# Kernel tuning notes

Measured on AMD Instinct MI355X. Metric: run time of the kernel, lower is better.

Reference implementation:

```python
import jax, jax.numpy as jnp
import numpy as np

B, N, D = 8, 2048, 16   # batch, n_points, n_dim (num_df == D)
K, DM = 32, 256         # k neighbors, d_model


def setup_inputs() -> dict:
    key = jax.random.key(0)
    k0, k1, k2, k3, k4, k5 = jax.random.split(key, 6)
    x = jax.random.normal(k0, (B, N, D), jnp.float32)
    features = jax.random.uniform(k1, (B, D), jnp.float32)
    # nn.Linear(k, d_model, bias=False) weights: [out, in] = [DM, K]
    lim = 1.0 / np.sqrt(K)
    W_crd = jax.random.uniform(k2, (DM, K), jnp.float32, -lim, lim)
    W_ftr = jax.random.uniform(k3, (DM, K), jnp.float32, -lim, lim)
    pe_crd = 0.01 * jax.random.normal(k4, (1, 1, D, DM), jnp.float32)
    pe_ftr = 0.01 * jax.random.normal(k5, (1, 1, D, DM), jnp.float32)
    return {"x": x, "features": features, "W_crd": W_crd, "W_ftr": W_ftr,
            "pe_crd": pe_crd, "pe_ftr": pe_ftr, "k": K}


def _forward(x, features, W_crd, W_ftr, pe_crd, pe_ftr, k):
    b, n, d = x.shape
    # split coordinates vs features per-dimension
    fmask = features[:, None, :] > 0.1                 # [B,1,D]
    x_crd = jnp.where(fmask, 0.0, x)                   # masked_fill(features_, 0)
    x_ftr = jnp.where(fmask, x, 0.0)                   # masked_fill(~features_, 0)
    xc = jnp.concatenate([x_crd, x_ftr], axis=-1)      # [B,N,2D]
    # masked stats with attn_mask=None -> plain mean / unbiased std over points
    mean = jnp.mean(xc, axis=1, keepdims=True)
    std = jnp.std(xc, axis=1, keepdims=True, ddof=1)
    xc = jnp.clip((xc - mean) / (std + 1e-5), -10.0, 10.0)
    # pairwise L2 distances on coordinate part (torch.cdist, p=2)
    sq = jnp.sum(x_crd * x_crd, axis=-1)               # [B,N]
    d2 = sq[:, :, None] + sq[:, None, :] - 2.0 * jnp.einsum('bnd,bmd->bnm', x_crd, x_crd)
    dist = jnp.sqrt(jnp.maximum(d2, 0.0))              # [B,N,N]
    # k nearest neighbors (smallest distance, self included)
    _, idx = jax.lax.top_k(-dist, k)                   # [B,N,k]
    nb = xc[jnp.arange(b)[:, None, None], idx]         # gather neighbors [B,N,k,2D]
    local = nb - xc[:, :, None, :]                     # project_local: center frame
    xk = jnp.transpose(local, (0, 1, 3, 2))            # flatten=False -> [B,N,2D,k]
    crd, ftr = xk[:, :, :d, :], xk[:, :, d:, :]
    o_crd = (jnp.einsum('bnpk,dk->bnpd', crd, W_crd) + pe_crd).sum(axis=2)
    o_ftr = (jnp.einsum('bnpk,dk->bnpd', ftr, W_ftr) + pe_ftr).sum(axis=2)
    pe_loss = jnp.abs(pe_crd).sum() + jnp.abs(pe_ftr).sum()
    # dropout is identity in eval mode
    return o_crd + o_ftr, pe_loss


def reference(x, features, W_crd, W_ftr, pe_crd, pe_ftr, k):
    return _forward(x, features, W_crd, W_ftr, pe_crd, pe_ftr, k)
```

## Files before the change

### kernel.cpp

```cpp
#include <hip/hip_runtime.h>
#include <stdint.h>

#define B 8
#define N 2048
#define D 16
#define KNN 32
#define DM 256
#define CAP 128

__global__ __launch_bounds__(256) void knn_prep(
    const float* __restrict__ x, const float* __restrict__ features,
    const float* __restrict__ Wc, const float* __restrict__ Wf,
    const float* __restrict__ pec, const float* __restrict__ pef,
    float* __restrict__ xcrdT, float* __restrict__ sq,
    float* __restrict__ Tc, float* __restrict__ Tf,
    float* __restrict__ WcT, float* __restrict__ WfT,
    float* __restrict__ cbias, float* __restrict__ pe_loss_out)
{
    if (blockIdx.x == 64) {
        int dm = threadIdx.x;
        float cb = 0.f, al = 0.f;
#pragma unroll
        for (int p = 0; p < D; ++p)
            cb += pec[p * DM + dm] + pef[p * DM + dm];
#pragma unroll
        for (int p = 0; p < D; ++p)
            al += fabsf(pec[p * DM + dm]) + fabsf(pef[p * DM + dm]);
        cbias[dm] = cb;
#pragma unroll
        for (int k = 0; k < KNN; ++k) {
            WcT[k * DM + dm] = Wc[dm * KNN + k];
            WfT[k * DM + dm] = Wf[dm * KNN + k];
        }
        __shared__ float redf[256];
        redf[dm] = al; __syncthreads();
        for (int st = 128; st > 0; st >>= 1) {
            if (dm < st) redf[dm] += redf[dm + st];
            __syncthreads();
        }
        if (dm == 0) pe_loss_out[0] = redf[0];
        return;
    }

    int tid = threadIdx.x;
    int b = blockIdx.x >> 3;

    double ls[D], lq[D];
#pragma unroll
    for (int d = 0; d < D; ++d) { ls[d] = 0.0; lq[d] = 0.0; }
    for (int r = 0; r < 8; ++r) {
        const float* row = x + ((size_t)b * N + r * 256 + tid) * D;
#pragma unroll
        for (int d = 0; d < D; d += 4) {
            float4 v = *(const float4*)(row + d);
            double x0 = v.x, x1 = v.y, x2 = v.z, x3 = v.w;
            ls[d]   += x0; lq[d]   += x0 * x0;
            ls[d+1] += x1; lq[d+1] += x1 * x1;
            ls[d+2] += x2; lq[d+2] += x2 * x2;
            ls[d+3] += x3; lq[d+3] += x3 * x3;
        }
    }
#pragma unroll
    for (int d = 0; d < D; ++d) {
        double s = ls[d], q = lq[d];
#pragma unroll
        for (int st = 32; st >= 1; st >>= 1) {
            s += __shfl_xor(s, st, 64);
            q += __shfl_xor(q, st, 64);
        }
        ls[d] = s; lq[d] = q;
    }
    __shared__ double sred[4][2 * D];
    __shared__ float smean[32], sscale[32];
    int wave = tid >> 6, lane = tid & 63;
    if (lane == 0) {
#pragma unroll
        for (int d = 0; d < D; ++d) {
            sred[wave][d]     = ls[d];
            sred[wave][D + d] = lq[d];
        }
    }
    __syncthreads();
    if (tid < D) {
        int d = tid;
        double S = sred[0][d] + sred[1][d] + sred[2][d] + sred[3][d];
        double Q = sred[0][D+d] + sred[1][D+d] + sred[2][D+d] + sred[3][D+d];
        double mean = S / (double)N;
        double var  = (Q - S * S / (double)N) / (double)(N - 1);
        if (var < 0.0) var = 0.0;
        float stdv = (float)sqrt(var);
        float scl  = 1.0f / (stdv + 1e-5f);
        float scl0 = 1.0f / (0.0f + 1e-5f);
        bool mask = features[b * D + d] > 0.1f;
        smean [d]      = mask ? 0.0f : (float)mean;
        sscale[d]      = mask ? scl0 : scl;
        smean [16 + d] = mask ? (float)mean : 0.0f;
        sscale[16 + d] = mask ? scl : scl0;
    }
    __syncthreads();

    int t = blockIdx.x * 256 + tid;
    int nn = t & (N - 1);
    float tc = 0.f, tf = 0.f, s = 0.f;
    float row[D];
#pragma unroll
    for (int d = 0; d < D; ++d) {
        float xv = x[(size_t)t * D + d];
        bool mask = features[b * D + d] > 0.1f;
        float xc = mask ? 0.f : xv;
        float xf = mask ? xv : 0.f;
        row[d] = xc;
        s += xc * xc;
        float vc = (xc - smean[d])      * sscale[d];
        vc = fminf(10.f, fmaxf(-10.f, vc));
        float vf = (xf - smean[16 + d]) * sscale[16 + d];
        vf = fminf(10.f, fmaxf(-10.f, vf));
        tc += vc; tf += vf;
    }
#pragma unroll
    for (int d = 0; d < D; ++d)
        xcrdT[((size_t)b * D + d) * N + nn] = row[d];
    sq[t] = s; Tc[t] = tc; Tf[t] = tf;
}

#define WAVE_LDS_FENCE() do {                                   \
    asm volatile("s_waitcnt lgkmcnt(0)" ::: "memory");          \
    __builtin_amdgcn_sched_barrier(0);                          \
} while (0)

__global__ __launch_bounds__(256) void knn_main(
    const float* __restrict__ xcrdT, const float* __restrict__ sq,
    const float* __restrict__ Tc, const float* __restrict__ Tf,
    const float* __restrict__ WcT, const float* __restrict__ WfT,
    const float* __restrict__ cbias, float* __restrict__ out)
{
    __shared__ float tile[D][256];
    __shared__ unsigned long long collect[8][CAP];
    __shared__ int sortedm[8][KNN];
    __shared__ float akbk[8][KNN][2];

    const int tid  = threadIdx.x;
    const int lane = tid & 63;
    const int wid  = tid >> 6;
    const int qid0 = blockIdx.x * 8 + wid * 2;
    const int b  = qid0 >> 11;
    const int n0 = qid0 & (N - 1);
    const int n1 = n0 + 1;
    const int c0 = wid * 2, c1 = c0 + 1;

    const float* xbT = xcrdT + (size_t)b * D * N;
    const float* sqb = sq + b * N;

    float qx0[D], qx1[D];
#pragma unroll
    for (int d = 0; d < D; ++d) {
        float2 v = *(const float2*)(xbT + (size_t)d * N + n0);
        qx0[d] = v.x; qx1[d] = v.y;
    }
    const float sqn0 = sqb[n0], sqn1 = sqb[n1];

    float orig0[KNN], orig1[KNN];
    float vm0 = 1e30f, vm1 = 1e30f;
#pragma unroll
    for (int t = 0; t < 8; ++t) {
        __syncthreads();
        {
            const float* src = xbT + (size_t)(wid * 4) * N + t * 256 + lane * 4;
#pragma unroll
            for (int dd = 0; dd < 4; ++dd) {
                float4 v = *(const float4*)(src + (size_t)dd * N);
                *(float4*)&tile[wid * 4 + dd][lane * 4] = v;
            }
        }
        __syncthreads();
#pragma unroll
        for (int jt = 0; jt < 4; ++jt) {
            const int j  = t * 4 + jt;
            const int ml = jt * 64 + lane;
            float dot0 = 0.f, dot1 = 0.f;
#pragma unroll
            for (int d = 0; d < D; ++d) {
                float v = tile[d][ml];
                dot0 += qx0[d] * v;
                dot1 += qx1[d] * v;
            }
            float sm = sqb[t * 256 + ml];
            float o0 = fabsf(sqrtf(fmaxf(sqn0 + sm - 2.0f * dot0, 0.f)));
            float o1 = fabsf(sqrtf(fmaxf(sqn1 + sm - 2.0f * dot1, 0.f)));
            orig0[j] = o0; orig1[j] = o1;
            vm0 = fminf(vm0, o0); vm1 = fminf(vm1, o1);
        }
    }

#pragma unroll
    for (int k = 2; k <= 64; k <<= 1) {
#pragma unroll
        for (int j = k >> 1; j >= 1; j >>= 1) {
            float o0 = __shfl_xor(vm0, j, 64);
            float o1 = __shfl_xor(vm1, j, 64);
            bool lower = (lane & j) == 0;
            bool up    = (lane & k) == 0;
            vm0 = (lower == up) ? fminf(vm0, o0) : fmaxf(vm0, o0);
            vm1 = (lower == up) ? fminf(vm1, o1) : fmaxf(vm1, o1);
        }
    }
    const float tau0 = __shfl(vm0, 31, 64);
    const float tau1 = __shfl(vm1, 31, 64);

    const unsigned long long lmask = (1ULL << lane) - 1ULL;
    int T0, T1;
    {
        int base = 0;
#pragma unroll
        for (int j = 0; j < KNN; ++j) {
            bool f = (orig0[j] <= tau0);
            unsigned long long mk = __ballot(f);
            if (f) {
                int pos = base + (int)__popcll(mk & lmask);
                if (pos < CAP)
                    collect[c0][pos] =
                        (((unsigned long long)__float_as_uint(orig0[j])) << 11)
                        | (unsigned)(j * 64 + lane);
            }
            base += (int)__popcll(mk);
        }
        T0 = base < CAP ? base : CAP;
    }
    {
        int base = 0;
#pragma unroll
        for (int j = 0; j < KNN; ++j) {
            bool f = (orig1[j] <= tau1);
            unsigned long long mk = __ballot(f);
            if (f) {
                int pos = base + (int)__popcll(mk & lmask);
                if (pos < CAP)
                    collect[c1][pos] =
                        (((unsigned long long)__float_as_uint(orig1[j])) << 11)
                        | (unsigned)(j * 64 + lane);
            }
            base += (int)__popcll(mk);
        }
        T1 = base < CAP ? base : CAP;
    }
    WAVE_LDS_FENCE();

    if (T0 <= 64 && T1 <= 64) {
        unsigned long long key0 = (lane < T0) ? collect[c0][lane] : ~0ULL;
        unsigned long long key1 = (lane < T1) ? collect[c1][lane] : ~0ULL;
#pragma unroll
        for (int k = 2; k <= 64; k <<= 1) {
#pragma unroll
            for (int j = k >> 1; j >= 1; j >>= 1) {
                unsigned long long o0 = __shfl_xor(key0, j, 64);
                unsigned long long o1 = __shfl_xor(key1, j, 64);
                bool lower = (lane & j) == 0;
                bool up    = (lane & k) == 0;
                unsigned long long mn0 = (o0 < key0) ? o0 : key0;
                unsigned long long mx0 = (o0 < key0) ? key0 : o0;
                unsigned long long mn1 = (o1 < key1) ? o1 : key1;
                unsigned long long mx1 = (o1 < key1) ? key1 : o1;
                key0 = (lower == up) ? mn0 : mx0;
                key1 = (lower == up) ? mn1 : mx1;
            }
        }
        if (lane < KNN) {
            sortedm[c0][lane] = (int)(key0 & 2047u);
            sortedm[c1][lane] = (int)(key1 & 2047u);
        }
    } else {
#pragma unroll 1
        for (int q = 0; q < 2; ++q) {
            int T = q ? T1 : T0;
            unsigned long long* co = collect[q ? c1 : c0];
            int* so = sortedm[q ? c1 : c0];
            if (T <= 64) {
                unsigned long long key = (lane < T) ? co[lane] : ~0ULL;
#pragma unroll
                for (int k = 2; k <= 64; k <<= 1) {
#pragma unroll
                    for (int j = k >> 1; j >= 1; j >>= 1) {
                        unsigned long long o = __shfl_xor(key, j, 64);
                        bool lower = (lane & j) == 0;
                        bool up    = (lane & k) == 0;
                        unsigned long long mn = (o < key) ? o : key;
                        unsigned long long mx = (o < key) ? key : o;
                        key = (lower == up) ? mn : mx;
                    }
                }
                if (lane < KNN) so[lane] = (int)(key & 2047u);
            } else {
#pragma unroll 1
                for (int slot = 0; slot < CAP / 64; ++slot) {
                    int i = lane + slot * 64;
                    if (i < T) {
                        unsigned long long mk = co[i];
                        int rank = 0;
#pragma unroll 4
                        for (int t2 = 0; t2 < T; ++t2)
                            rank += (co[t2] < mk) ? 1 : 0;
                        if (rank < KNN) so[rank] = (int)(mk & 2047u);
                    }
                }
            }
        }
    }
    WAVE_LDS_FENCE();

    const float* Tcb = Tc + b * N;
    const float* Tfb = Tf + b * N;
    {
        const float Tcn0 = Tcb[n0], Tfn0 = Tfb[n0];
        const float Tcn1 = Tcb[n1], Tfn1 = Tfb[n1];
        int q = lane >> 5;
        int k = lane & 31;
        int wm = sortedm[c0 + q][k];
        float av = Tcb[wm] - (q ? Tcn1 : Tcn0);
        float bv = Tfb[wm] - (q ? Tfn1 : Tfn0);
        akbk[c0 + q][k][0] = av;
        akbk[c0 + q][k][1] = bv;
    }
    WAVE_LDS_FENCE();

    float acc0[4] = {0.f, 0.f, 0.f, 0.f};
    float acc1[4] = {0.f, 0.f, 0.f, 0.f};

#pragma unroll
    for (int k = 0; k < KNN; ++k) {
        float ak0 = akbk[c0][k][0], bk0 = akbk[c0][k][1];
        float ak1 = akbk[c1][k][0], bk1 = akbk[c1][k][1];
        const float* wc = WcT + k * DM + lane;
        const float* wf = WfT + k * DM + lane;
#pragma unroll
        for (int q = 0; q < 4; ++q) {
            float wcv = wc[q * 64];
            float wfv = wf[q * 64];
            acc0[q] += wcv * ak0 + wfv * bk0;
            acc1[q] += wcv * ak1 + wfv * bk1;
        }
    }

    size_t ob0 = (size_t)qid0 * DM + lane;
#pragma unroll
    for (int q = 0; q < 4; ++q) {
        float cb = cbias[lane + q * 64];
        out[ob0 + q * 64]      = acc0[q] + cb;
        out[ob0 + DM + q * 64] = acc1[q] + cb;
    }
}

extern "C" void kernel_launch(void* const* d_in, const int* in_sizes, int n_in,
                              void* d_out, int out_size, void* d_ws, size_t ws_size,
                              hipStream_t stream)
{
    const float* x        = (const float*)d_in[0];
    const float* features = (const float*)d_in[1];
    const float* W_crd    = (const float*)d_in[2];
    const float* W_ftr    = (const float*)d_in[3];
    const float* pe_crd   = (const float*)d_in[4];
    const float* pe_ftr   = (const float*)d_in[5];

    float* out = (float*)d_out;

    float* xcrdT = (float*)d_ws;
    float* sqv   = xcrdT + (size_t)B * N * D;
    float* Tc    = sqv  + B * N;
    float* Tf    = Tc   + B * N;
    float* cbias = Tf   + B * N;
    float* WcT   = cbias + DM;
    float* WfT   = WcT + KNN * DM;

    knn_prep<<<65, 256, 0, stream>>>(x, features, W_crd, W_ftr, pe_crd, pe_ftr,
                                     xcrdT, sqv, Tc, Tf, WcT, WfT, cbias,
                                     out + (size_t)out_size - 1);
    knn_main<<<(B * N) / 8, 256, 0, stream>>>(xcrdT, sqv, Tc, Tf,
                                              WcT, WfT, cbias, out);
}
```

Measured before the change: 165.3 us.

## Double-buffer distance tile loads through registers and stage squared norms in LDS

The coordinate tile loop now uses two 128-column LDS buffers. The next tile's global loads are issued into registers before computing on the current tile, then written to the other buffer, so each step needs one barrier instead of two. The per-column squared norms are also staged in LDS instead of being read from global memory inside the compute loop. The price is more loop iterations (16 instead of 8), each with a barrier, plus extra live registers holding the prefetched data.

```diff
diff --git a/kernel.cpp b/kernel.cpp
--- a/kernel.cpp
+++ b/kernel.cpp
@@ -134,7 +134,8 @@
     const float* __restrict__ WcT, const float* __restrict__ WfT,
     const float* __restrict__ cbias, float* __restrict__ out)
 {
-    __shared__ float tile[D][256];
+    __shared__ float tbuf[2][D][128];
+    __shared__ float sqt[2][128];
     __shared__ unsigned long long collect[8][CAP];
     __shared__ int sortedm[8][KNN];
     __shared__ float akbk[8][KNN][2];
@@ -159,37 +160,52 @@
     }
     const float sqn0 = sqb[n0], sqn1 = sqb[n1];
 
+    const int d0 = tid >> 5;
+    const int cc = tid & 31;
+    float4 rA, rB, rS;
+
+#define STAGE_ISSUE(ht) do {                                            \
+    const float* src_ = xbT + (size_t)d0 * N + (ht) * 128 + cc * 4;     \
+    rA = *(const float4*)(src_);                                        \
+    rB = *(const float4*)(src_ + (size_t)8 * N);                        \
+    if (tid < 32) rS = *(const float4*)(sqb + (ht) * 128 + tid * 4);    \
+} while (0)
+
+#define STAGE_WRITE(ht) do {                                            \
+    *(float4*)&tbuf[(ht) & 1][d0][cc * 4] = rA;                         \
+    *(float4*)&tbuf[(ht) & 1][d0 + 8][cc * 4] = rB;                     \
+    if (tid < 32) *(float4*)&sqt[(ht) & 1][tid * 4] = rS;               \
+} while (0)
+
     float orig0[KNN], orig1[KNN];
     float vm0 = 1e30f, vm1 = 1e30f;
-#pragma unroll
-    for (int t = 0; t < 8; ++t) {
-        __syncthreads();
-        {
-            const float* src = xbT + (size_t)(wid * 4) * N + t * 256 + lane * 4;
-#pragma unroll
-            for (int dd = 0; dd < 4; ++dd) {
-                float4 v = *(const float4*)(src + (size_t)dd * N);
-                *(float4*)&tile[wid * 4 + dd][lane * 4] = v;
-            }
-        }
-        __syncthreads();
-#pragma unroll
-        for (int jt = 0; jt < 4; ++jt) {
-            const int j  = t * 4 + jt;
+
+    STAGE_ISSUE(0);
+    STAGE_WRITE(0);
+    __syncthreads();
+
+#pragma unroll
+    for (int ht = 0; ht < 16; ++ht) {
+        if (ht + 1 < 16) STAGE_ISSUE(ht + 1);
+#pragma unroll
+        for (int jt = 0; jt < 2; ++jt) {
+            const int j  = ht * 2 + jt;
             const int ml = jt * 64 + lane;
             float dot0 = 0.f, dot1 = 0.f;
 #pragma unroll
             for (int d = 0; d < D; ++d) {
-                float v = tile[d][ml];
+                float v = tbuf[ht & 1][d][ml];
                 dot0 += qx0[d] * v;
                 dot1 += qx1[d] * v;
             }
-            float sm = sqb[t * 256 + ml];
+            float sm = sqt[ht & 1][ml];
             float o0 = fabsf(sqrtf(fmaxf(sqn0 + sm - 2.0f * dot0, 0.f)));
             float o1 = fabsf(sqrtf(fmaxf(sqn1 + sm - 2.0f * dot1, 0.f)));
             orig0[j] = o0; orig1[j] = o1;
             vm0 = fminf(vm0, o0); vm1 = fminf(vm1, o1);
         }
+        if (ht + 1 < 16) STAGE_WRITE(ht + 1);
+        __syncthreads();
     }
 
 #pragma unroll
```

Result: slower. 298.9 us (+80.8%).
